# Kernel tuning notes

Hardware: AMD Instinct MI355X
Metric: run time of the kernel (lower is better)

The kernel has to match this reference:

```python
import jax, jax.numpy as jnp
import numpy as np

N_NODES = 100000
N_EDGES = 1600000
D_IN = 128
D_HID = 128
D_OUT = 32


def setup_inputs() -> dict:
    key = jax.random.key(0)
    ks = jax.random.split(key, 10)
    x = jax.random.normal(ks[0], (N_NODES, D_IN), dtype=jnp.float32)
    edge_index = jax.random.randint(ks[1], (2, N_EDGES), 0, N_NODES, dtype=jnp.int64)
    s = 0.05
    return {
        "x": x,
        "edge_index": edge_index,
        "Wl0": jax.random.normal(ks[2], (D_IN, D_HID), jnp.float32) * s,
        "bl0": jnp.zeros((D_HID,), jnp.float32),
        "Wr0": jax.random.normal(ks[3], (D_IN, D_HID), jnp.float32) * s,
        "Wl1": jax.random.normal(ks[4], (D_HID, D_HID), jnp.float32) * s,
        "bl1": jnp.zeros((D_HID,), jnp.float32),
        "Wr1": jax.random.normal(ks[5], (D_HID, D_HID), jnp.float32) * s,
        "Wl2": jax.random.normal(ks[6], (D_HID, D_OUT), jnp.float32) * s,
        "bl2": jnp.zeros((D_OUT,), jnp.float32),
        "Wr2": jax.random.normal(ks[7], (D_HID, D_OUT), jnp.float32) * s,
    }


def _sage_conv(x, src, dst, Wl, bl, Wr):
    # PyG SAGEConv (aggr='mean', root_weight=True):
    # out[i] = lin_l(mean_{j in N(i)} x_j) + lin_r(x_i)
    n = x.shape[0]
    msgs = x[src]                                        # [E, F] gather
    agg = jax.ops.segment_sum(msgs, dst, num_segments=n) # [N, F] scatter-add
    deg = jax.ops.segment_sum(jnp.ones((src.shape[0],), x.dtype), dst, num_segments=n)
    mean = agg / jnp.maximum(deg, 1.0)[:, None]
    return mean @ Wl + bl + x @ Wr


def reference(x, edge_index, Wl0, bl0, Wr0, Wl1, bl1, Wr1, Wl2, bl2, Wr2):
    src, dst = edge_index[0], edge_index[1]
    h = jax.nn.relu(_sage_conv(x, src, dst, Wl0, bl0, Wr0))
    h = jax.nn.relu(_sage_conv(h, src, dst, Wl1, bl1, Wr1))
    h = _sage_conv(h, src, dst, Wl2, bl2, Wr2)
    return jax.nn.log_softmax(h, axis=1)
```

## Files before the change

kernel.cpp:

```cpp
#include <hip/hip_runtime.h>
#include <hip/hip_bf16.h>
#include <math.h>

#define NN 100000
#define NE 1600000

#define NCB 391
#define EB  8192
#define SCT 512
#define HBK 64
#define NSB 196
#define WPB 144

typedef __attribute__((ext_vector_type(8))) short short8;
typedef __attribute__((ext_vector_type(4))) float f32x4;

__device__ __forceinline__ unsigned short f2bf(float f) {
  union { float f; unsigned int i; } v; v.f = f;
  unsigned int i = v.i;
  unsigned int r = (i + 0x7FFFu + ((i >> 16) & 1u)) >> 16;
  return (unsigned short)r;
}
__device__ __forceinline__ float bflo(unsigned int u) {
  union { unsigned int i; float f; } v; v.i = u << 16; return v.f;
}
__device__ __forceinline__ float bfhi(unsigned int u) {
  union { unsigned int i; float f; } v; v.i = u & 0xFFFF0000u; return v.f;
}
__device__ __forceinline__ float bf1(unsigned short u) {
  union { unsigned int i; float f; } v; v.i = ((unsigned int)u) << 16; return v.f;
}

__global__ __launch_bounds__(512) void k_prep(
    const int* __restrict__ dst, int* __restrict__ part,
    const float* __restrict__ Wl0, const float* __restrict__ Wr0,
    const float* __restrict__ Wl1, const float* __restrict__ Wr1,
    const float* __restrict__ Wl2, const float* __restrict__ Wr2,
    unsigned short* __restrict__ B0, unsigned short* __restrict__ B1,
    unsigned short* __restrict__ B2) {
  if (blockIdx.x < HBK) {
    __shared__ int h[NCB];
    for (int i = threadIdx.x; i < NCB; i += 512) h[i] = 0;
    __syncthreads();
    int stride = HBK * 512;
    for (int e = blockIdx.x * 512 + threadIdx.x; e < NE; e += stride) {
      int d = dst[e];
      d = d < 0 ? 0 : (d >= NN ? NN - 1 : d);
      atomicAdd(&h[d >> 8], 1);
    }
    __syncthreads();
    for (int i = threadIdx.x; i < NCB; i += 512) part[blockIdx.x * NCB + i] = h[i];
  } else {
    int idx = (blockIdx.x - HBK) * 512 + threadIdx.x;
    if (idx < 32768) {
      int n = idx >> 7, k = idx & 127;
      float v = (n < 128) ? Wl0[k * 128 + n] : Wr0[k * 128 + (n - 128)];
      B0[idx] = f2bf(v);
    } else if (idx < 65536) {
      int j = idx - 32768;
      int n = j >> 7, k = j & 127;
      float v = (n < 128) ? Wl1[k * 128 + n] : Wr1[k * 128 + (n - 128)];
      B1[j] = f2bf(v);
    } else if (idx < 73728) {
      int j = idx - 65536;
      int n = j >> 7, k = j & 127;
      float v = (n < 32) ? Wl2[k * 32 + n] : Wr2[k * 32 + (n - 32)];
      B2[j] = f2bf(v);
    }
  }
}

__global__ __launch_bounds__(512) void k_cscan(const int* __restrict__ part,
                                               int* __restrict__ cboff,
                                               int* __restrict__ ccur,
                                               int* __restrict__ csroff) {
  __shared__ int sd[512];
  int t = threadIdx.x;
  int v = 0;
  if (t < NCB) {
    int s0 = 0, s1 = 0, s2 = 0, s3 = 0;
    #pragma unroll 4
    for (int k = 0; k < HBK; k += 4) {
      s0 += part[(k + 0) * NCB + t];
      s1 += part[(k + 1) * NCB + t];
      s2 += part[(k + 2) * NCB + t];
      s3 += part[(k + 3) * NCB + t];
    }
    v = (s0 + s1) + (s2 + s3);
    ccur[t] = 0;
  }
  sd[t] = v;
  __syncthreads();
  for (int st = 1; st < 512; st <<= 1) {
    int x = (t >= st) ? sd[t - st] : 0;
    __syncthreads();
    sd[t] += x;
    __syncthreads();
  }
  if (t < NCB) cboff[t] = sd[t] - v;
  if (t == NCB - 1) { cboff[NCB] = sd[t]; csroff[NN] = sd[t]; }
}


__device__ __forceinline__ void cscatter_body(
    char* smem, int bid,
    const int* __restrict__ src, const int* __restrict__ dst,
    const int* __restrict__ cboff, int* __restrict__ ccur,
    unsigned int* __restrict__ ebuf) {
  int* lh = (int*)smem;
  unsigned int* sRank = (unsigned int*)(smem + 1600);
  unsigned int* sPay  = (unsigned int*)(smem + 1600 + EB * 4);
  int t = threadIdx.x;
  int base = bid * EB;
  for (int i = t; i < NCB; i += SCT) lh[i] = 0;
  __syncthreads();
  #pragma unroll
  for (int i = 0; i < EB / SCT; i++) {
    int idx = i * SCT + t;
    int e = base + idx;
    unsigned int rk = 0xFFFFFFFFu, pv = 0;
    if (e < NE) {
      int d = dst[e];
      d = d < 0 ? 0 : (d >= NN ? NN - 1 : d);
      int s = src[e];
      s = s < 0 ? 0 : (s >= NN ? NN - 1 : s);
      int cb = d >> 8;
      int r = atomicAdd(&lh[cb], 1);
      rk = (((unsigned int)cb) << 13) | (unsigned int)r;
      pv = (((unsigned int)(d & 255)) << 17) | (unsigned int)s;
    }
    sRank[idx] = rk;
    sPay[idx]  = pv;
  }
  __syncthreads();
  for (int i = t; i < NCB; i += SCT) {
    int c = lh[i];
    int g = c ? atomicAdd(&ccur[i], c) : 0;
    lh[i] = cboff[i] + g;
  }
  __syncthreads();
  #pragma unroll
  for (int i = 0; i < EB / SCT; i++) {
    int idx = i * SCT + t;
    unsigned int rk = sRank[idx];
    if (rk != 0xFFFFFFFFu) {
      int cb = rk >> 13;
      int r  = rk & 0x1FFF;
      ebuf[lh[cb] + r] = sPay[idx];
    }
  }
}

__device__ __forceinline__ void mgemm0_body(
    char* smem, int bid, const float* __restrict__ A,
    const unsigned short* __restrict__ Bp, const float* __restrict__ bias,
    unsigned short* __restrict__ yl, unsigned short* __restrict__ yr) {
  unsigned short* sA = (unsigned short*)smem;
  int tid = threadIdx.x;
  int nb  = bid * 128;

  #pragma unroll
  for (int i = 0; i < 8; i++) {
    int j = i * 512 + tid;
    int m = j >> 5;
    int k4 = (j & 31) * 4;
    int gn = nb + m;
    float4 v = make_float4(0.f, 0.f, 0.f, 0.f);
    if (gn < NN) v = *(const float4*)&A[gn * 128 + k4];
    unsigned int p0 = (unsigned int)f2bf(v.x) | ((unsigned int)f2bf(v.y) << 16);
    unsigned int p1 = (unsigned int)f2bf(v.z) | ((unsigned int)f2bf(v.w) << 16);
    *(uint2*)&sA[m * 136 + k4] = make_uint2(p0, p1);
  }
  __syncthreads();

  int wave = tid >> 6, lane = tid & 63;
  int l15 = lane & 15, lq = lane >> 4;
  int wm = wave & 1, wn = wave >> 1;
  int mbase = wm * 64;
  int nbase = wn * 64;

  f32x4 acc[4][4];
  #pragma unroll
  for (int mi = 0; mi < 4; mi++)
    #pragma unroll
    for (int ni = 0; ni < 4; ni++) acc[mi][ni] = (f32x4){0.f, 0.f, 0.f, 0.f};

  #pragma unroll
  for (int kc = 0; kc < 4; kc++) {
    int k0 = kc * 32 + lq * 8;
    short8 af[4], bfr[4];
    #pragma unroll
    for (int ni = 0; ni < 4; ni++)
      bfr[ni] = *(const short8*)&Bp[(nbase + ni * 16 + l15) * 128 + k0];
    #pragma unroll
    for (int mi = 0; mi < 4; mi++)
      af[mi] = *(const short8*)&sA[(mbase + mi * 16 + l15) * 136 + k0];
    #pragma unroll
    for (int mi = 0; mi < 4; mi++)
      #pragma unroll
      for (int ni = 0; ni < 4; ni++)
        acc[mi][ni] = __builtin_amdgcn_mfma_f32_16x16x32_bf16(
            af[mi], bfr[ni], acc[mi][ni], 0, 0, 0);
  }

  #pragma unroll
  for (int mi = 0; mi < 4; mi++) {
    #pragma unroll
    for (int ni = 0; ni < 4; ni++) {
      int n = nbase + ni * 16 + l15;
      #pragma unroll
      for (int r = 0; r < 4; r++) {
        int gn = nb + mbase + mi * 16 + lq * 4 + r;
        if (gn < NN) {
          float v = acc[mi][ni][r];
          if (n < 128) {
            yl[(size_t)gn * 128 + n] = f2bf(v);
          } else {
            int n2 = n - 128;
            yr[(size_t)gn * 128 + n2] = f2bf(v + bias[n2]);
          }
        }
      }
    }
  }
}

__global__ __launch_bounds__(512) void k_scatgemm(
    const int* __restrict__ src, const int* __restrict__ dst,
    const int* __restrict__ cboff, int* __restrict__ ccur,
    unsigned int* __restrict__ ebuf,
    const float* __restrict__ x, const unsigned short* __restrict__ B0,
    const float* __restrict__ bias,
    unsigned short* __restrict__ yl, unsigned short* __restrict__ yr) {
  __shared__ char smem[1600 + EB * 8];
  if (blockIdx.x < NSB) {
    cscatter_body(smem, blockIdx.x, src, dst, cboff, ccur, ebuf);
  } else {
    mgemm0_body(smem, blockIdx.x - NSB, x, B0, bias, yl, yr);
  }
}

__global__ __launch_bounds__(256) void k_crefine(
    const unsigned int* __restrict__ ebuf, const int* __restrict__ cboff,
    int* __restrict__ csroff, float* __restrict__ invd,
    int* __restrict__ csrsrc) {
  __shared__ int lh[256], pos[256], cur[256];
  int b = blockIdx.x, t = threadIdx.x;
  lh[t] = 0; cur[t] = 0;
  __syncthreads();
  int beg = cboff[b], end = cboff[b + 1];
  for (int i = beg + t; i < end; i += 256) atomicAdd(&lh[ebuf[i] >> 17], 1);
  __syncthreads();
  int v = lh[t];
  pos[t] = v;
  __syncthreads();
  for (int st = 1; st < 256; st <<= 1) {
    int x = (t >= st) ? pos[t - st] : 0;
    __syncthreads();
    pos[t] += x;
    __syncthreads();
  }
  int nid = b * 256 + t;
  int mybase = cboff[b] + pos[t] - v;
  if (nid < NN) {
    csroff[nid] = mybase;
    invd[nid] = 1.0f / (float)(v < 1 ? 1 : v);
  }
  __syncthreads();
  pos[t] = mybase;
  __syncthreads();
  for (int i = beg + t; i < end; i += 256) {
    unsigned int u = ebuf[i];
    int local = u >> 17;
    int r = atomicAdd(&cur[local], 1);
    csrsrc[pos[local] + r] = (int)(u & 0x1FFFFu);
  }
}

template <int NC>
__global__ __launch_bounds__(512) void k_mgemm(
    const unsigned short* __restrict__ A, const unsigned short* __restrict__ Bp,
    const float* __restrict__ bias,
    unsigned short* __restrict__ yl, unsigned short* __restrict__ yr) {
  __shared__ unsigned short sA[128 * 136];
  int tid = threadIdx.x;
  int nb  = blockIdx.x * 128;

  #pragma unroll
  for (int i = 0; i < 4; i++) {
    int j = i * 512 + tid;
    int m = j >> 4;
    int k8 = (j & 15) * 8;
    int gn = nb + m;
    uint4 v = make_uint4(0, 0, 0, 0);
    if (gn < NN) v = *(const uint4*)&A[gn * 128 + k8];
    *(uint4*)&sA[m * 136 + k8] = v;
  }
  __syncthreads();

  int wave = tid >> 6, lane = tid & 63;
  int l15 = lane & 15, lq = lane >> 4;
  constexpr int MT = (NC == 256) ? 4 : 2;
  constexpr int NT = (NC == 256) ? 4 : 2;
  int wm, wn;
  if (NC == 256) { wm = wave & 1; wn = wave >> 1; }
  else           { wm = wave >> 1; wn = wave & 1; }
  int mbase = wm * (MT * 16);
  int nbase = wn * (NT * 16);

  f32x4 acc[MT][NT];
  #pragma unroll
  for (int mi = 0; mi < MT; mi++)
    #pragma unroll
    for (int ni = 0; ni < NT; ni++) acc[mi][ni] = (f32x4){0.f, 0.f, 0.f, 0.f};

  #pragma unroll
  for (int kc = 0; kc < 4; kc++) {
    int k0 = kc * 32 + lq * 8;
    short8 af[MT], bfr[NT];
    #pragma unroll
    for (int ni = 0; ni < NT; ni++)
      bfr[ni] = *(const short8*)&Bp[(nbase + ni * 16 + l15) * 128 + k0];
    #pragma unroll
    for (int mi = 0; mi < MT; mi++)
      af[mi] = *(const short8*)&sA[(mbase + mi * 16 + l15) * 136 + k0];
    #pragma unroll
    for (int mi = 0; mi < MT; mi++)
      #pragma unroll
      for (int ni = 0; ni < NT; ni++)
        acc[mi][ni] = __builtin_amdgcn_mfma_f32_16x16x32_bf16(
            af[mi], bfr[ni], acc[mi][ni], 0, 0, 0);
  }

  constexpr int HC = NC / 2;
  #pragma unroll
  for (int mi = 0; mi < MT; mi++) {
    #pragma unroll
    for (int ni = 0; ni < NT; ni++) {
      int n = nbase + ni * 16 + l15;
      #pragma unroll
      for (int r = 0; r < 4; r++) {
        int gn = nb + mbase + mi * 16 + lq * 4 + r;
        if (gn < NN) {
          float v = acc[mi][ni][r];
          if (n < HC) {
            yl[(size_t)gn * HC + n] = f2bf(v);
          } else {
            int n2 = n - HC;
            yr[(size_t)gn * HC + n2] = f2bf(v + bias[n2]);
          }
        }
      }
    }
  }
}

__global__ __launch_bounds__(256) void k_agg128(
    const unsigned short* __restrict__ yl, const unsigned short* __restrict__ yr,
    const int* __restrict__ off, const int* __restrict__ csr,
    const float* __restrict__ invd, unsigned short* __restrict__ out, int relu) {
  int wid  = (blockIdx.x * 256 + threadIdx.x) >> 6;
  int lane = threadIdx.x & 63;
  if (wid >= NN) return;
  int beg = off[wid], end = off[wid + 1];
  const unsigned int* ylp = (const unsigned int*)yl;
  float ax0 = 0.f, ay0 = 0.f, ax1 = 0.f, ay1 = 0.f;
  float ax2 = 0.f, ay2 = 0.f, ax3 = 0.f, ay3 = 0.f;
  int e = beg;
  for (; e + 7 < end; e += 8) {
    int s0 = csr[e],     s1 = csr[e + 1], s2 = csr[e + 2], s3 = csr[e + 3];
    int s4 = csr[e + 4], s5 = csr[e + 5], s6 = csr[e + 6], s7 = csr[e + 7];
    unsigned int u0 = ylp[s0 * 64 + lane];
    unsigned int u1 = ylp[s1 * 64 + lane];
    unsigned int u2 = ylp[s2 * 64 + lane];
    unsigned int u3 = ylp[s3 * 64 + lane];
    unsigned int u4 = ylp[s4 * 64 + lane];
    unsigned int u5 = ylp[s5 * 64 + lane];
    unsigned int u6 = ylp[s6 * 64 + lane];
    unsigned int u7 = ylp[s7 * 64 + lane];
    ax0 += bflo(u0); ay0 += bfhi(u0);
    ax1 += bflo(u1); ay1 += bfhi(u1);
    ax2 += bflo(u2); ay2 += bfhi(u2);
    ax3 += bflo(u3); ay3 += bfhi(u3);
    ax0 += bflo(u4); ay0 += bfhi(u4);
    ax1 += bflo(u5); ay1 += bfhi(u5);
    ax2 += bflo(u6); ay2 += bfhi(u6);
    ax3 += bflo(u7); ay3 += bfhi(u7);
  }
  for (; e < end; e++) {
    int s = csr[e];
    unsigned int u = ylp[s * 64 + lane];
    ax0 += bflo(u); ay0 += bfhi(u);
  }
  float sc = invd[wid];
  unsigned int rv = ((const unsigned int*)yr)[wid * 64 + lane];
  float vx = ((ax0 + ax1) + (ax2 + ax3)) * sc + bflo(rv);
  float vy = ((ay0 + ay1) + (ay2 + ay3)) * sc + bfhi(rv);
  if (relu) { vx = fmaxf(vx, 0.f); vy = fmaxf(vy, 0.f); }
  ((unsigned int*)out)[wid * 64 + lane] =
      (unsigned int)f2bf(vx) | ((unsigned int)f2bf(vy) << 16);
}

__global__ __launch_bounds__(256) void k_agg32_lsm(
    const unsigned short* __restrict__ yl, const unsigned short* __restrict__ yr,
    const int* __restrict__ off, const int* __restrict__ csr,
    const float* __restrict__ invd, float* __restrict__ out) {
  int row  = (blockIdx.x * 256 + threadIdx.x) >> 5;
  int lane = threadIdx.x & 31;
  if (row >= NN) return;
  int beg = off[row], end = off[row + 1];
  float a0 = 0.f, a1 = 0.f, a2 = 0.f, a3 = 0.f;
  int e = beg;
  for (; e + 3 < end; e += 4) {
    int s0 = csr[e], s1 = csr[e + 1], s2 = csr[e + 2], s3 = csr[e + 3];
    a0 += bf1(yl[s0 * 32 + lane]);
    a1 += bf1(yl[s1 * 32 + lane]);
    a2 += bf1(yl[s2 * 32 + lane]);
    a3 += bf1(yl[s3 * 32 + lane]);
  }
  for (; e < end; e++) a0 += bf1(yl[csr[e] * 32 + lane]);
  float v = ((a0 + a1) + (a2 + a3)) * invd[row] + bf1(yr[row * 32 + lane]);
  float m = v;
  #pragma unroll
  for (int o = 16; o; o >>= 1) m = fmaxf(m, __shfl_xor(m, o, 32));
  float ex = expf(v - m);
  float s = ex;
  #pragma unroll
  for (int o = 16; o; o >>= 1) s += __shfl_xor(s, o, 32);
  out[row * 32 + lane] = v - m - logf(s);
}


extern "C" void kernel_launch(void* const* d_in, const int* in_sizes, int n_in,
                              void* d_out, int out_size, void* d_ws, size_t ws_size,
                              hipStream_t stream) {
  (void)in_sizes; (void)n_in; (void)out_size; (void)ws_size;
  const float* x   = (const float*)d_in[0];
  const int*   ei  = (const int*)d_in[1];
  const float* Wl0 = (const float*)d_in[2];
  const float* bl0 = (const float*)d_in[3];
  const float* Wr0 = (const float*)d_in[4];
  const float* Wl1 = (const float*)d_in[5];
  const float* bl1 = (const float*)d_in[6];
  const float* Wr1 = (const float*)d_in[7];
  const float* Wl2 = (const float*)d_in[8];
  const float* bl2 = (const float*)d_in[9];
  const float* Wr2 = (const float*)d_in[10];
  const int* srcI = ei;
  const int* dstI = ei + NE;

  char* w = (char*)d_ws;
  int*   ccur   = (int*)(w + (16 << 10));
  int*   cboff  = (int*)(w + (32 << 10));
  unsigned short* B0 = (unsigned short*)(w + (64 << 10));
  unsigned short* B1 = (unsigned short*)(w + (160 << 10));
  unsigned short* B2 = (unsigned short*)(w + (256 << 10));
  int*   part   = (int*)(w + (288 << 10));
  int*   csroff = (int*)(w + (512 << 10));
  float* invd   = (float*)(w + (1024 << 10));
  unsigned int* ebuf = (unsigned int*)(w + (size_t)(2) * 1024 * 1024);
  int*   csrsrc = (int*)(w + (size_t)(9) * 1024 * 1024);
  unsigned short* ylb = (unsigned short*)(w + (size_t)(16) * 1024 * 1024);
  unsigned short* yrb = (unsigned short*)(w + (size_t)(48) * 1024 * 1024);
  unsigned short* hb  = (unsigned short*)(w + (size_t)(80) * 1024 * 1024);

  dim3 gg((NN + 127) / 128);

  k_prep<<<HBK + WPB, 512, 0, stream>>>(dstI, part, Wl0, Wr0, Wl1, Wr1, Wl2, Wr2,
                                        B0, B1, B2);
  k_cscan<<<1, 512, 0, stream>>>(part, cboff, ccur, csroff);
  k_scatgemm<<<NSB + 782, 512, 0, stream>>>(srcI, dstI, cboff, ccur, ebuf,
                                            x, B0, bl0, ylb, yrb);
  k_crefine<<<NCB, 256, 0, stream>>>(ebuf, cboff, csroff, invd, csrsrc);
  k_agg128<<<(NN * 64) / 256, 256, 0, stream>>>(ylb, yrb, csroff, csrsrc, invd, hb, 1);
  k_mgemm<256><<<gg, 512, 0, stream>>>(hb, B1, bl1, ylb, yrb);
  k_agg128<<<(NN * 64) / 256, 256, 0, stream>>>(ylb, yrb, csroff, csrsrc, invd, hb, 1);
  k_mgemm<64><<<gg, 512, 0, stream>>>(hb, B2, bl2, ylb, yrb);
  k_agg32_lsm<<<(NN * 32) / 256, 256, 0, stream>>>(ylb, yrb, csroff, csrsrc, invd,
                                                   (float*)d_out);
}
```

Baseline: 450.7 us.

## Fuse neighbor aggregation into following GEMM via shared-memory staging

The separate 128-wide aggregation kernel and the following MFMA GEMM are merged into one kernel. Each block aggregates its 128 nodes (8 waves, 16 nodes each) directly into the shared-memory A tile, then runs the GEMM. This removes the round trip of the hidden activation through global memory and one launch per layer. Outputs now ping-pong between two yl/yr buffer pairs to avoid read/write hazards. The trade-off is less parallelism in the gather phase, since each wave handles 16 rows serially and the GEMM waits on the slowest wave in the block.

After: 601.4 us. 1.33x slower.

```diff
diff --git a/kernel.cpp b/kernel.cpp
--- a/kernel.cpp
+++ b/kernel.cpp
@@ -101,7 +101,6 @@
   if (t == NCB - 1) { cboff[NCB] = sd[t]; csroff[NN] = sd[t]; }
 }
 
-
 __device__ __forceinline__ void cscatter_body(
     char* smem, int bid,
     const int* __restrict__ src, const int* __restrict__ dst,
@@ -278,27 +277,64 @@
 }
 
 template <int NC>
-__global__ __launch_bounds__(512) void k_mgemm(
-    const unsigned short* __restrict__ A, const unsigned short* __restrict__ Bp,
-    const float* __restrict__ bias,
-    unsigned short* __restrict__ yl, unsigned short* __restrict__ yr) {
+__global__ __launch_bounds__(512) void k_aggmm(
+    const unsigned short* __restrict__ yl, const unsigned short* __restrict__ yr,
+    const int* __restrict__ off, const int* __restrict__ csr,
+    const float* __restrict__ invd,
+    const unsigned short* __restrict__ Bp, const float* __restrict__ bias,
+    unsigned short* __restrict__ oyl, unsigned short* __restrict__ oyr) {
   __shared__ unsigned short sA[128 * 136];
   int tid = threadIdx.x;
   int nb  = blockIdx.x * 128;
-
-  #pragma unroll
-  for (int i = 0; i < 4; i++) {
-    int j = i * 512 + tid;
-    int m = j >> 4;
-    int k8 = (j & 15) * 8;
-    int gn = nb + m;
-    uint4 v = make_uint4(0, 0, 0, 0);
-    if (gn < NN) v = *(const uint4*)&A[gn * 128 + k8];
-    *(uint4*)&sA[m * 136 + k8] = v;
-  }
-  __syncthreads();
-
   int wave = tid >> 6, lane = tid & 63;
+  const unsigned int* ylp = (const unsigned int*)yl;
+  const unsigned int* yrp = (const unsigned int*)yr;
+
+  for (int q = 0; q < 16; q++) {
+    int m = wave * 16 + q;
+    int wid = nb + m;
+    float vx = 0.f, vy = 0.f;
+    if (wid < NN) {
+      int beg = off[wid], end = off[wid + 1];
+      float ax0 = 0.f, ay0 = 0.f, ax1 = 0.f, ay1 = 0.f;
+      float ax2 = 0.f, ay2 = 0.f, ax3 = 0.f, ay3 = 0.f;
+      int e = beg;
+      for (; e + 7 < end; e += 8) {
+        int s0 = csr[e],     s1 = csr[e + 1], s2 = csr[e + 2], s3 = csr[e + 3];
+        int s4 = csr[e + 4], s5 = csr[e + 5], s6 = csr[e + 6], s7 = csr[e + 7];
+        unsigned int u0 = ylp[s0 * 64 + lane];
+        unsigned int u1 = ylp[s1 * 64 + lane];
+        unsigned int u2 = ylp[s2 * 64 + lane];
+        unsigned int u3 = ylp[s3 * 64 + lane];
+        unsigned int u4 = ylp[s4 * 64 + lane];
+        unsigned int u5 = ylp[s5 * 64 + lane];
+        unsigned int u6 = ylp[s6 * 64 + lane];
+        unsigned int u7 = ylp[s7 * 64 + lane];
+        ax0 += bflo(u0); ay0 += bfhi(u0);
+        ax1 += bflo(u1); ay1 += bfhi(u1);
+        ax2 += bflo(u2); ay2 += bfhi(u2);
+        ax3 += bflo(u3); ay3 += bfhi(u3);
+        ax0 += bflo(u4); ay0 += bfhi(u4);
+        ax1 += bflo(u5); ay1 += bfhi(u5);
+        ax2 += bflo(u6); ay2 += bfhi(u6);
+        ax3 += bflo(u7); ay3 += bfhi(u7);
+      }
+      for (; e < end; e++) {
+        int s = csr[e];
+        unsigned int u = ylp[s * 64 + lane];
+        ax0 += bflo(u); ay0 += bfhi(u);
+      }
+      float sc = invd[wid];
+      unsigned int rv = yrp[wid * 64 + lane];
+      vx = ((ax0 + ax1) + (ax2 + ax3)) * sc + bflo(rv);
+      vy = ((ay0 + ay1) + (ay2 + ay3)) * sc + bfhi(rv);
+      vx = fmaxf(vx, 0.f); vy = fmaxf(vy, 0.f);
+    }
+    *(unsigned int*)&sA[m * 136 + 2 * lane] =
+        (unsigned int)f2bf(vx) | ((unsigned int)f2bf(vy) << 16);
+  }
+  __syncthreads();
+
   int l15 = lane & 15, lq = lane >> 4;
   constexpr int MT = (NC == 256) ? 4 : 2;
   constexpr int NT = (NC == 256) ? 4 : 2;
@@ -344,61 +380,15 @@
         if (gn < NN) {
           float v = acc[mi][ni][r];
           if (n < HC) {
-            yl[(size_t)gn * HC + n] = f2bf(v);
+            oyl[(size_t)gn * HC + n] = f2bf(v);
           } else {
             int n2 = n - HC;
-            yr[(size_t)gn * HC + n2] = f2bf(v + bias[n2]);
+            oyr[(size_t)gn * HC + n2] = f2bf(v + bias[n2]);
           }
         }
       }
     }
   }
-}
-
-__global__ __launch_bounds__(256) void k_agg128(
-    const unsigned short* __restrict__ yl, const unsigned short* __restrict__ yr,
-    const int* __restrict__ off, const int* __restrict__ csr,
-    const float* __restrict__ invd, unsigned short* __restrict__ out, int relu) {
-  int wid  = (blockIdx.x * 256 + threadIdx.x) >> 6;
-  int lane = threadIdx.x & 63;
-  if (wid >= NN) return;
-  int beg = off[wid], end = off[wid + 1];
-  const unsigned int* ylp = (const unsigned int*)yl;
-  float ax0 = 0.f, ay0 = 0.f, ax1 = 0.f, ay1 = 0.f;
-  float ax2 = 0.f, ay2 = 0.f, ax3 = 0.f, ay3 = 0.f;
-  int e = beg;
-  for (; e + 7 < end; e += 8) {
-    int s0 = csr[e],     s1 = csr[e + 1], s2 = csr[e + 2], s3 = csr[e + 3];
-    int s4 = csr[e + 4], s5 = csr[e + 5], s6 = csr[e + 6], s7 = csr[e + 7];
-    unsigned int u0 = ylp[s0 * 64 + lane];
-    unsigned int u1 = ylp[s1 * 64 + lane];
-    unsigned int u2 = ylp[s2 * 64 + lane];
-    unsigned int u3 = ylp[s3 * 64 + lane];
-    unsigned int u4 = ylp[s4 * 64 + lane];
-    unsigned int u5 = ylp[s5 * 64 + lane];
-    unsigned int u6 = ylp[s6 * 64 + lane];
-    unsigned int u7 = ylp[s7 * 64 + lane];
-    ax0 += bflo(u0); ay0 += bfhi(u0);
-    ax1 += bflo(u1); ay1 += bfhi(u1);
-    ax2 += bflo(u2); ay2 += bfhi(u2);
-    ax3 += bflo(u3); ay3 += bfhi(u3);
-    ax0 += bflo(u4); ay0 += bfhi(u4);
-    ax1 += bflo(u5); ay1 += bfhi(u5);
-    ax2 += bflo(u6); ay2 += bfhi(u6);
-    ax3 += bflo(u7); ay3 += bfhi(u7);
-  }
-  for (; e < end; e++) {
-    int s = csr[e];
-    unsigned int u = ylp[s * 64 + lane];
-    ax0 += bflo(u); ay0 += bfhi(u);
-  }
-  float sc = invd[wid];
-  unsigned int rv = ((const unsigned int*)yr)[wid * 64 + lane];
-  float vx = ((ax0 + ax1) + (ax2 + ax3)) * sc + bflo(rv);
-  float vy = ((ay0 + ay1) + (ay2 + ay3)) * sc + bfhi(rv);
-  if (relu) { vx = fmaxf(vx, 0.f); vy = fmaxf(vy, 0.f); }
-  ((unsigned int*)out)[wid * 64 + lane] =
-      (unsigned int)f2bf(vx) | ((unsigned int)f2bf(vy) << 16);
 }
 
 __global__ __launch_bounds__(256) void k_agg32_lsm(
@@ -460,9 +450,10 @@
   float* invd   = (float*)(w + (1024 << 10));
   unsigned int* ebuf = (unsigned int*)(w + (size_t)(2) * 1024 * 1024);
   int*   csrsrc = (int*)(w + (size_t)(9) * 1024 * 1024);
-  unsigned short* ylb = (unsigned short*)(w + (size_t)(16) * 1024 * 1024);
-  unsigned short* yrb = (unsigned short*)(w + (size_t)(48) * 1024 * 1024);
-  unsigned short* hb  = (unsigned short*)(w + (size_t)(80) * 1024 * 1024);
+  unsigned short* ylA = (unsigned short*)(w + (size_t)(16)  * 1024 * 1024);
+  unsigned short* yrA = (unsigned short*)(w + (size_t)(48)  * 1024 * 1024);
+  unsigned short* ylB = (unsigned short*)(w + (size_t)(80)  * 1024 * 1024);
+  unsigned short* yrB = (unsigned short*)(w + (size_t)(112) * 1024 * 1024);
 
   dim3 gg((NN + 127) / 128);
 
@@ -470,12 +461,12 @@
                                         B0, B1, B2);
   k_cscan<<<1, 512, 0, stream>>>(part, cboff, ccur, csroff);
   k_scatgemm<<<NSB + 782, 512, 0, stream>>>(srcI, dstI, cboff, ccur, ebuf,
-                                            x, B0, bl0, ylb, yrb);
+                                            x, B0, bl0, ylA, yrA);
   k_crefine<<<NCB, 256, 0, stream>>>(ebuf, cboff, csroff, invd, csrsrc);
-  k_agg128<<<(NN * 64) / 256, 256, 0, stream>>>(ylb, yrb, csroff, csrsrc, invd, hb, 1);
-  k_mgemm<256><<<gg, 512, 0, stream>>>(hb, B1, bl1, ylb, yrb);
-  k_agg128<<<(NN * 64) / 256, 256, 0, stream>>>(ylb, yrb, csroff, csrsrc, invd, hb, 1);
-  k_mgemm<64><<<gg, 512, 0, stream>>>(hb, B2, bl2, ylb, yrb);
-  k_agg32_lsm<<<(NN * 32) / 256, 256, 0, stream>>>(ylb, yrb, csroff, csrsrc, invd,
+  k_aggmm<256><<<gg, 512, 0, stream>>>(ylA, yrA, csroff, csrsrc, invd,
+                                       B1, bl1, ylB, yrB);
+  k_aggmm<64><<<gg, 512, 0, stream>>>(ylB, yrB, csroff, csrsrc, invd,
+                                      B2, bl2, ylA, yrA);
+  k_agg32_lsm<<<(NN * 32) / 256, 256, 0, stream>>>(ylA, yrA, csroff, csrsrc, invd,
                                                    (float*)d_out);
 }
```

## Halve scatter edge block, atomically reduce histogram, widen refine blocks

Applied to the files above, without the earlier changes.

The coarse-bucket histogram is now reduced with global atomics into a zeroed counter array (memset added) instead of writing per-block partials that the scan kernel summed. The scatter phase uses twice as many blocks with half the edges each, which shrinks the shared-memory footprint of the fused scatter/GEMM kernel to the GEMM tile size and may raise occupancy. The refine kernel moves to 512 threads per block to stride edges faster. These changes trade an extra memset launch and global atomics for a lighter scan and better parallelism in the scatter and refine steps.

New measurement: 452.6 us. About the same (+0.4%).

```diff
diff --git a/kernel.cpp b/kernel.cpp
--- a/kernel.cpp
+++ b/kernel.cpp
@@ -6,10 +6,10 @@
 #define NE 1600000
 
 #define NCB 391
-#define EB  8192
+#define EB  4096
 #define SCT 512
 #define HBK 64
-#define NSB 196
+#define NSB 391
 #define WPB 144
 
 typedef __attribute__((ext_vector_type(8))) short short8;
@@ -32,7 +32,7 @@
 }
 
 __global__ __launch_bounds__(512) void k_prep(
-    const int* __restrict__ dst, int* __restrict__ part,
+    const int* __restrict__ dst, int* __restrict__ bcnt,
     const float* __restrict__ Wl0, const float* __restrict__ Wr0,
     const float* __restrict__ Wl1, const float* __restrict__ Wr1,
     const float* __restrict__ Wl2, const float* __restrict__ Wr2,
@@ -49,7 +49,10 @@
       atomicAdd(&h[d >> 8], 1);
     }
     __syncthreads();
-    for (int i = threadIdx.x; i < NCB; i += 512) part[blockIdx.x * NCB + i] = h[i];
+    for (int i = threadIdx.x; i < NCB; i += 512) {
+      int v = h[i];
+      if (v) atomicAdd(&bcnt[i], v);
+    }
   } else {
     int idx = (blockIdx.x - HBK) * 512 + threadIdx.x;
     if (idx < 32768) {
@@ -70,25 +73,12 @@
   }
 }
 
-__global__ __launch_bounds__(512) void k_cscan(const int* __restrict__ part,
+__global__ __launch_bounds__(512) void k_cscan(const int* __restrict__ bcnt,
                                                int* __restrict__ cboff,
-                                               int* __restrict__ ccur,
                                                int* __restrict__ csroff) {
   __shared__ int sd[512];
   int t = threadIdx.x;
-  int v = 0;
-  if (t < NCB) {
-    int s0 = 0, s1 = 0, s2 = 0, s3 = 0;
-    #pragma unroll 4
-    for (int k = 0; k < HBK; k += 4) {
-      s0 += part[(k + 0) * NCB + t];
-      s1 += part[(k + 1) * NCB + t];
-      s2 += part[(k + 2) * NCB + t];
-      s3 += part[(k + 3) * NCB + t];
-    }
-    v = (s0 + s1) + (s2 + s3);
-    ccur[t] = 0;
-  }
+  int v = (t < NCB) ? bcnt[t] : 0;
   sd[t] = v;
   __syncthreads();
   for (int st = 1; st < 512; st <<= 1) {
@@ -100,7 +90,6 @@
   if (t < NCB) cboff[t] = sd[t] - v;
   if (t == NCB - 1) { cboff[NCB] = sd[t]; csroff[NN] = sd[t]; }
 }
-
 
 __device__ __forceinline__ void cscatter_body(
     char* smem, int bid,
@@ -232,7 +221,7 @@
     const float* __restrict__ x, const unsigned short* __restrict__ B0,
     const float* __restrict__ bias,
     unsigned short* __restrict__ yl, unsigned short* __restrict__ yr) {
-  __shared__ char smem[1600 + EB * 8];
+  __shared__ char smem[128 * 136 * 2];
   if (blockIdx.x < NSB) {
     cscatter_body(smem, blockIdx.x, src, dst, cboff, ccur, ebuf);
   } else {
@@ -240,36 +229,37 @@
   }
 }
 
-__global__ __launch_bounds__(256) void k_crefine(
+__global__ __launch_bounds__(512) void k_crefine(
     const unsigned int* __restrict__ ebuf, const int* __restrict__ cboff,
     int* __restrict__ csroff, float* __restrict__ invd,
     int* __restrict__ csrsrc) {
   __shared__ int lh[256], pos[256], cur[256];
   int b = blockIdx.x, t = threadIdx.x;
-  lh[t] = 0; cur[t] = 0;
+  if (t < 256) { lh[t] = 0; cur[t] = 0; }
   __syncthreads();
   int beg = cboff[b], end = cboff[b + 1];
-  for (int i = beg + t; i < end; i += 256) atomicAdd(&lh[ebuf[i] >> 17], 1);
-  __syncthreads();
-  int v = lh[t];
-  pos[t] = v;
+  for (int i = beg + t; i < end; i += 512) atomicAdd(&lh[ebuf[i] >> 17], 1);
+  __syncthreads();
+  int v = (t < 256) ? lh[t] : 0;
+  if (t < 256) pos[t] = v;
   __syncthreads();
   for (int st = 1; st < 256; st <<= 1) {
-    int x = (t >= st) ? pos[t - st] : 0;
-    __syncthreads();
-    pos[t] += x;
-    __syncthreads();
-  }
-  int nid = b * 256 + t;
-  int mybase = cboff[b] + pos[t] - v;
-  if (nid < NN) {
-    csroff[nid] = mybase;
-    invd[nid] = 1.0f / (float)(v < 1 ? 1 : v);
-  }
-  __syncthreads();
-  pos[t] = mybase;
-  __syncthreads();
-  for (int i = beg + t; i < end; i += 256) {
+    int x = (t >= st && t < 256) ? pos[t - st] : 0;
+    __syncthreads();
+    if (t < 256) pos[t] += x;
+    __syncthreads();
+  }
+  if (t < 256) {
+    int nid = b * 256 + t;
+    int mybase = cboff[b] + pos[t] - v;
+    if (nid < NN) {
+      csroff[nid] = mybase;
+      invd[nid] = 1.0f / (float)(v < 1 ? 1 : v);
+    }
+    pos[t] = mybase;
+  }
+  __syncthreads();
+  for (int i = beg + t; i < end; i += 512) {
     unsigned int u = ebuf[i];
     int local = u >> 17;
     int r = atomicAdd(&cur[local], 1);
@@ -450,12 +440,12 @@
   const int* dstI = ei + NE;
 
   char* w = (char*)d_ws;
-  int*   ccur   = (int*)(w + (16 << 10));
+  int*   bcnt   = (int*)(w + 0);
+  int*   ccur   = (int*)(w + (4 << 10));
   int*   cboff  = (int*)(w + (32 << 10));
   unsigned short* B0 = (unsigned short*)(w + (64 << 10));
   unsigned short* B1 = (unsigned short*)(w + (160 << 10));
   unsigned short* B2 = (unsigned short*)(w + (256 << 10));
-  int*   part   = (int*)(w + (288 << 10));
   int*   csroff = (int*)(w + (512 << 10));
   float* invd   = (float*)(w + (1024 << 10));
   unsigned int* ebuf = (unsigned int*)(w + (size_t)(2) * 1024 * 1024);
@@ -466,12 +456,13 @@
 
   dim3 gg((NN + 127) / 128);
 
-  k_prep<<<HBK + WPB, 512, 0, stream>>>(dstI, part, Wl0, Wr0, Wl1, Wr1, Wl2, Wr2,
+  hipMemsetAsync(w, 0, 8 << 10, stream);
+  k_prep<<<HBK + WPB, 512, 0, stream>>>(dstI, bcnt, Wl0, Wr0, Wl1, Wr1, Wl2, Wr2,
                                         B0, B1, B2);
-  k_cscan<<<1, 512, 0, stream>>>(part, cboff, ccur, csroff);
+  k_cscan<<<1, 512, 0, stream>>>(bcnt, cboff, csroff);
   k_scatgemm<<<NSB + 782, 512, 0, stream>>>(srcI, dstI, cboff, ccur, ebuf,
                                             x, B0, bl0, ylb, yrb);
-  k_crefine<<<NCB, 256, 0, stream>>>(ebuf, cboff, csroff, invd, csrsrc);
+  k_crefine<<<NCB, 512, 0, stream>>>(ebuf, cboff, csroff, invd, csrsrc);
   k_agg128<<<(NN * 64) / 256, 256, 0, stream>>>(ylb, yrb, csroff, csrsrc, invd, hb, 1);
   k_mgemm<256><<<gg, 512, 0, stream>>>(hb, B1, bl1, ylb, yrb);
   k_agg128<<<(NN * 64) / 256, 256, 0, stream>>>(ylb, yrb, csroff, csrsrc, invd, hb, 1);
```
